# Kernel optimization log

Measured on AMD Instinct MI355X. Metric: run time of the kernel, lower is better.

## Reference

```python
import jax, jax.numpy as jnp
import numpy as np

B, N, C = 4, 2048, 64   # batch, tokens, num_feat
HS = 512                # hidden_size
H = HS // C             # 8 heads, head_dim = C = 64
EPS = 1e-6


def _ln(x, g, b):
    m = x.mean(-1, keepdims=True)
    v = ((x - m) ** 2).mean(-1, keepdims=True)
    return (x - m) / jnp.sqrt(v + EPS) * g + b


def setup_inputs() -> dict:
    key = jax.random.key(0)
    ks = jax.random.split(key, 8)
    s = 0.02
    return {
        "x": jax.random.normal(ks[0], (B, N, C), jnp.float32),
        "g1": jnp.ones((C,), jnp.float32),
        "be1": jnp.zeros((C,), jnp.float32),
        "Wqkv": jax.random.normal(ks[1], (C, 3 * HS), jnp.float32) * s,
        "bqkv": jnp.zeros((3 * HS,), jnp.float32),
        "Wout": jax.random.normal(ks[2], (HS, C), jnp.float32) * s,
        "bout": jnp.zeros((C,), jnp.float32),
        "g2": jnp.ones((C,), jnp.float32),
        "be2": jnp.zeros((C,), jnp.float32),
        "W1": jax.random.normal(ks[3], (C, HS // 8), jnp.float32) * s,
        "b1": jax.random.normal(ks[4], (HS // 8,), jnp.float32) * 1e-6,
        "W2": jax.random.normal(ks[5], (HS // 8, C), jnp.float32) * s,
        "b2": jax.random.normal(ks[6], (C,), jnp.float32) * 1e-6,
    }


def reference(x, g1, be1, Wqkv, bqkv, Wout, bout, g2, be2, W1, b1, W2, b2):
    b_, n_, c_ = x.shape
    hs = Wout.shape[0]
    h_ = hs // c_
    res = x
    y = _ln(x, g1, be1)
    # fused QKV: (B,N,3*HS) -> (3,B,H,N,D) with D = c_
    qkv = (y @ Wqkv + bqkv).reshape(b_, n_, 3, h_, c_).transpose(2, 0, 3, 1, 4)
    q, k, v = qkv[0], qkv[1], qkv[2]
    scores = jnp.einsum('bhqd,bhkd->bhqk', q, k) / jnp.sqrt(jnp.asarray(c_, x.dtype))
    probs = jax.nn.softmax(scores, axis=-1)
    ctx = jnp.einsum('bhqk,bhkd->bhqd', probs, v)
    ctx = ctx.transpose(0, 2, 1, 3).reshape(b_, n_, hs)
    attn = jax.nn.gelu(ctx @ Wout + bout, approximate=False)  # GELU after out proj per source
    x2 = attn + res
    y2 = _ln(x2, g2, be2)
    mlp = jax.nn.gelu(y2 @ W1 + b1, approximate=False) @ W2 + b2
    return mlp + x2
```

## Files before the change

kernel.cpp:

```cpp
#include <hip/hip_runtime.h>


#define NN 2048
#define CC 64
#define HH 8
#define HSZ 512
#define QKSCALE 0.42466092f

typedef __bf16 bf16x8 __attribute__((ext_vector_type(8)));
typedef float f32x4 __attribute__((ext_vector_type(4)));

__device__ __forceinline__ float b2f(unsigned short u) {
  union { unsigned int i; float f; } v; v.i = ((unsigned int)u) << 16; return v.f;
}
__device__ __forceinline__ unsigned short f2b(float f) {
  union { float f; unsigned int i; } v; v.f = f;
  unsigned int r = v.i + 0x7FFFu + ((v.i >> 16) & 1u);
  return (unsigned short)(r >> 16);
}
__device__ __forceinline__ unsigned int pk2(float a, float b) {
  return (unsigned int)f2b(a) | ((unsigned int)f2b(b) << 16);
}
__device__ __forceinline__ unsigned char f2fp8(float f) {
  int p = __builtin_amdgcn_cvt_pk_fp8_f32(f, f, 0, false);
  return (unsigned char)(p & 0xFF);
}
__device__ __forceinline__ float gelu_f(float x) {
  return 0.5f * x * (1.0f + erff(x * 0.7071067811865475f));
}

__global__ __launch_bounds__(256) void k_ln_qkv(
    const float* __restrict__ x,
    const float* __restrict__ g1,
    const float* __restrict__ be1,
    const float* __restrict__ W,
    const float* __restrict__ bqkv,
    unsigned char* __restrict__ Qb,
    unsigned char* __restrict__ Kb,
    unsigned char* __restrict__ VbT)
{
  __shared__ __align__(16) unsigned short As[64 * 72];
  __shared__ __align__(16) unsigned short Ws[128 * 72];
  const int tid = threadIdx.x, wv = tid >> 6, lane = tid & 63;
  const int col = lane & 15, quad = lane >> 4;
  const int bm = blockIdx.x & 127, bn = blockIdx.x >> 7;
  const int m0 = bm * 64, nw = bn * 128;

  const int c4 = tid & 15;
  float4 gv = *(const float4*)(g1 + c4 * 4);
  float4 bv = *(const float4*)(be1 + c4 * 4);
  #pragma unroll
  for (int s = 0; s < 4; ++s) {
    int idx = s * 256 + tid;
    int row = idx >> 4;
    float4 xv = *(const float4*)(x + (size_t)(m0 + row) * CC + c4 * 4);
    float ps = xv.x + xv.y + xv.z + xv.w;
    float ps2 = xv.x * xv.x + xv.y * xv.y + xv.z * xv.z + xv.w * xv.w;
    #pragma unroll
    for (int off = 8; off; off >>= 1) {
      ps += __shfl_xor(ps, off, 16);
      ps2 += __shfl_xor(ps2, off, 16);
    }
    float mean = ps * (1.0f / 64.0f);
    float var = ps2 * (1.0f / 64.0f) - mean * mean;
    float rs = rsqrtf(var + 1e-6f);
    uint2 packed;
    packed.x = pk2((xv.x - mean) * rs * gv.x + bv.x, (xv.y - mean) * rs * gv.y + bv.y);
    packed.y = pk2((xv.z - mean) * rs * gv.z + bv.z, (xv.w - mean) * rs * gv.w + bv.w);
    *(uint2*)&As[row * 72 + c4 * 4] = packed;
  }

  {
    const int c_loc = tid & 127;
    const int kg = tid >> 7;
    const int ng = nw + c_loc;
    #pragma unroll
    for (int g = 0; g < 4; ++g) {
      float wv8[8];
      #pragma unroll
      for (int j = 0; j < 8; ++j) wv8[j] = W[(size_t)(kg * 32 + g * 8 + j) * 1536 + ng];
      uint4 u;
      u.x = pk2(wv8[0], wv8[1]); u.y = pk2(wv8[2], wv8[3]);
      u.z = pk2(wv8[4], wv8[5]); u.w = pk2(wv8[6], wv8[7]);
      *(uint4*)&Ws[c_loc * 72 + kg * 32 + g * 8] = u;
    }
  }
  __syncthreads();

  bf16x8 af0 = *(const bf16x8*)&As[(wv * 16 + col) * 72 + quad * 8];
  bf16x8 af1 = *(const bf16x8*)&As[(wv * 16 + col) * 72 + 32 + quad * 8];

  f32x4 acc[8];
  #pragma unroll
  for (int nt = 0; nt < 8; ++nt) acc[nt] = (f32x4){0.f, 0.f, 0.f, 0.f};
  #pragma unroll
  for (int nt = 0; nt < 8; ++nt) {
    bf16x8 b0 = *(const bf16x8*)&Ws[(nt * 16 + col) * 72 + quad * 8];
    bf16x8 b1 = *(const bf16x8*)&Ws[(nt * 16 + col) * 72 + 32 + quad * 8];
    acc[nt] = __builtin_amdgcn_mfma_f32_16x16x32_bf16(af0, b0, acc[nt], 0, 0, 0);
    acc[nt] = __builtin_amdgcn_mfma_f32_16x16x32_bf16(af1, b1, acc[nt], 0, 0, 0);
  }

  const int tkb = m0 + wv * 16 + quad * 4;
  const int bb = tkb >> 11;
  const int nnb = tkb & 2047;
  #pragma unroll
  for (int nt = 0; nt < 8; ++nt) {
    const int n0 = nw + nt * 16;
    const int which = n0 >> 9;
    const int h = (n0 >> 6) & 7;
    const int d0 = n0 & 63;
    const float bias = bqkv[n0 + col];
    float vv[4];
    #pragma unroll
    for (int r = 0; r < 4; ++r) vv[r] = acc[nt][r] + bias;
    if (which == 2) {
      int lo = __builtin_amdgcn_cvt_pk_fp8_f32(vv[0], vv[1], 0, false);
      int full = __builtin_amdgcn_cvt_pk_fp8_f32(vv[2], vv[3], lo, true);
      *(unsigned int*)(VbT + ((size_t)(bb * HH + h) * CC + d0 + col) * NN + nnb) =
          (unsigned int)full;
    } else {
      unsigned char* dst = (which == 0) ? Qb : Kb;
      #pragma unroll
      for (int r = 0; r < 4; ++r)
        dst[((size_t)(bb * HH + h) * NN + nnb + r) * CC + d0 + col] =
            f2fp8(vv[r] * QKSCALE);
    }
  }
}

__global__ __launch_bounds__(256) void k_attn(
    const unsigned char* __restrict__ Q,
    const unsigned char* __restrict__ K,
    const unsigned char* __restrict__ VT,
    const float* __restrict__ Wout,
    unsigned short* __restrict__ part,
    float* __restrict__ lsums)
{
  __shared__ __align__(16) unsigned char smem[27648];
  unsigned char* Ks = smem;
  unsigned char* Vt = smem + 5120;
  unsigned short* Wb = (unsigned short*)smem;
  unsigned short* Ob = (unsigned short*)(smem + 9216);
  const int tid = threadIdx.x, wv = tid >> 6, lane = tid & 63;
  const int col = lane & 15, quad = lane >> 4;
  const int bid = blockIdx.x;
  const int tc = bid & 1, qc = (bid >> 1) & 15, bh = bid >> 5;
  const size_t base = (size_t)bh * NN * CC;
  const int q0 = qc * 128 + wv * 32;
  const int t0 = tc * 1024;

  long qf[2][2];
  #pragma unroll
  for (int mt = 0; mt < 2; ++mt)
    #pragma unroll
    for (int kh = 0; kh < 2; ++kh)
      qf[mt][kh] = *(const long*)(Q + base + (size_t)(q0 + mt * 16 + col) * CC + kh * 32 + quad * 8);

  f32x4 o[2][4];
  #pragma unroll
  for (int mt = 0; mt < 2; ++mt)
    #pragma unroll
    for (int dt = 0; dt < 4; ++dt) o[mt][dt] = (f32x4){0.f, 0.f, 0.f, 0.f};
  float ls[2] = {0.f, 0.f};
  const int sl0 = ((quad & 1) << 5) + col;
  const int sl1 = sl0 + 16;
  const bool hiq = (quad >= 2);

  for (int kt = 0; kt < 16; ++kt) {
    const int tb = t0 + kt * 64;
    {
      int row = tid >> 2, c16 = (tid & 3) << 4;
      *(uint4*)&Ks[row * 80 + c16] = *(const uint4*)(K + base + (size_t)(tb + row) * CC + c16);
      *(uint4*)&Vt[row * 80 + c16] = *(const uint4*)(VT + base + (size_t)row * NN + tb + c16);
    }
    __syncthreads();

    unsigned int Dw[2][4];
    #pragma unroll
    for (int ct = 0; ct < 4; ++ct) {
      long k0 = *(const long*)&Ks[(ct * 16 + col) * 80 + quad * 8];
      long k1 = *(const long*)&Ks[(ct * 16 + col) * 80 + 32 + quad * 8];
      #pragma unroll
      for (int mt = 0; mt < 2; ++mt) {
        f32x4 a = (f32x4){0.f, 0.f, 0.f, 0.f};
        a = __builtin_amdgcn_mfma_f32_16x16x32_fp8_fp8(k0, qf[mt][0], a, 0, 0, 0);
        a = __builtin_amdgcn_mfma_f32_16x16x32_fp8_fp8(k1, qf[mt][1], a, 0, 0, 0);
        float p0 = exp2f(a[0]), p1 = exp2f(a[1]);
        float p2 = exp2f(a[2]), p3 = exp2f(a[3]);
        ls[mt] += (p0 + p1) + (p2 + p3);
        int lo = __builtin_amdgcn_cvt_pk_fp8_f32(p0, p1, 0, false);
        Dw[mt][ct] = (unsigned int)__builtin_amdgcn_cvt_pk_fp8_f32(p2, p3, lo, true);
      }
    }

    #pragma unroll
    for (int kh = 0; kh < 2; ++kh) {
      long pb[2];
      #pragma unroll
      for (int mt = 0; mt < 2; ++mt) {
        unsigned int a0 = (unsigned int)__shfl((int)Dw[mt][2 * kh], sl0, 64);
        unsigned int b0 = (unsigned int)__shfl((int)Dw[mt][2 * kh + 1], sl0, 64);
        unsigned int a1 = (unsigned int)__shfl((int)Dw[mt][2 * kh], sl1, 64);
        unsigned int b1 = (unsigned int)__shfl((int)Dw[mt][2 * kh + 1], sl1, 64);
        unsigned long lo = hiq ? b0 : a0;
        unsigned long hi = hiq ? b1 : a1;
        pb[mt] = (long)(lo | (hi << 32));
      }
      #pragma unroll
      for (int dt = 0; dt < 4; ++dt) {
        long vf = *(const long*)&Vt[(dt * 16 + col) * 80 + kh * 32 + quad * 8];
        o[0][dt] = __builtin_amdgcn_mfma_f32_16x16x32_fp8_fp8(vf, pb[0], o[0][dt], 0, 0, 0);
        o[1][dt] = __builtin_amdgcn_mfma_f32_16x16x32_fp8_fp8(vf, pb[1], o[1][dt], 0, 0, 0);
      }
    }
    __syncthreads();
  }

  const int h = bh & 7, b = bh >> 3;
  #pragma unroll
  for (int mt = 0; mt < 2; ++mt) {
    float v = ls[mt];
    v += __shfl_xor(v, 16, 64);
    v += __shfl_xor(v, 32, 64);
    if (quad == 0)
      lsums[(size_t)(tc * 32 + bh) * NN + q0 + mt * 16 + col] = v;
  }

  {
    const int c = tid & 63, kg = tid >> 6;
    #pragma unroll
    for (int j = 0; j < 16; ++j)
      Wb[c * 72 + kg * 16 + j] = f2b(Wout[(size_t)(h * 64 + kg * 16 + j) * 64 + c]);
  }
  unsigned short* Obw = Ob + wv * (32 * 72);
  #pragma unroll
  for (int mt = 0; mt < 2; ++mt)
    #pragma unroll
    for (int dt = 0; dt < 4; ++dt) {
      uint2 u;
      u.x = pk2(o[mt][dt][0], o[mt][dt][1]);
      u.y = pk2(o[mt][dt][2], o[mt][dt][3]);
      *(uint2*)&Obw[(mt * 16 + col) * 72 + dt * 16 + quad * 4] = u;
    }
  __syncthreads();

  #pragma unroll
  for (int mt = 0; mt < 2; ++mt) {
    bf16x8 oa0 = *(const bf16x8*)&Obw[(mt * 16 + col) * 72 + quad * 8];
    bf16x8 oa1 = *(const bf16x8*)&Obw[(mt * 16 + col) * 72 + 32 + quad * 8];
    #pragma unroll
    for (int nt = 0; nt < 4; ++nt) {
      bf16x8 bw0 = *(const bf16x8*)&Wb[(nt * 16 + col) * 72 + quad * 8];
      bf16x8 bw1 = *(const bf16x8*)&Wb[(nt * 16 + col) * 72 + 32 + quad * 8];
      f32x4 ac = (f32x4){0.f, 0.f, 0.f, 0.f};
      ac = __builtin_amdgcn_mfma_f32_16x16x32_bf16(oa0, bw0, ac, 0, 0, 0);
      ac = __builtin_amdgcn_mfma_f32_16x16x32_bf16(oa1, bw1, ac, 0, 0, 0);
      #pragma unroll
      for (int r = 0; r < 4; ++r) {
        int n = q0 + mt * 16 + quad * 4 + r;
        part[((size_t)(tc * 32 + bh) * NN + n) * CC + nt * 16 + col] = f2b(ac[r]);
      }
    }
  }
}

__global__ __launch_bounds__(256) void k_post(
    const unsigned short* __restrict__ part,
    const float* __restrict__ lsums,
    const float* __restrict__ x,
    const float* __restrict__ bout,
    const float* __restrict__ g2,
    const float* __restrict__ be2,
    const float* __restrict__ W1,
    const float* __restrict__ b1,
    const float* __restrict__ W2,
    const float* __restrict__ b2v,
    float* __restrict__ out)
{
  __shared__ __align__(16) float Ws1[64 * 64];
  __shared__ __align__(16) float Ws2[64 * 64];
  __shared__ float ys[4][64], hs[4][64];
  const int tid = threadIdx.x, wid = tid >> 6, lane = tid & 63;
  const int tk = blockIdx.x * 4 + wid;
  const int b = tk >> 11, n = tk & 2047;

  #pragma unroll
  for (int p = 0; p < 4; ++p) {
    int idx = p * 256 + tid;
    *(float4*)&Ws1[idx * 4] = *(const float4*)(W1 + idx * 4);
    *(float4*)&Ws2[idx * 4] = *(const float4*)(W2 + idx * 4);
  }

  float proj = 0.f;
  #pragma unroll
  for (int h = 0; h < 8; ++h) {
    size_t i0 = (size_t)(b * HH + h) * NN + n;
    size_t i1 = i0 + (size_t)32 * NN;
    float p = b2f(part[i0 * CC + lane]) + b2f(part[i1 * CC + lane]);
    float l = lsums[i0] + lsums[i1];
    proj += p * __builtin_amdgcn_rcpf(l);
  }

  float a = gelu_f(proj + bout[lane]);
  float x2 = a + x[(size_t)tk * CC + lane];
  float s = x2;
  #pragma unroll
  for (int off = 32; off; off >>= 1) s += __shfl_xor(s, off, 64);
  float mean = s * (1.0f / 64.0f);
  float d = x2 - mean;
  float vs = d * d;
  #pragma unroll
  for (int off = 32; off; off >>= 1) vs += __shfl_xor(vs, off, 64);
  float var = vs * (1.0f / 64.0f);
  ys[wid][lane] = d * rsqrtf(var + 1e-6f) * g2[lane] + be2[lane];
  __syncthreads();

  float acc2 = 0.f;
  #pragma unroll 8
  for (int c = 0; c < 64; ++c) acc2 += ys[wid][c] * Ws1[c * 64 + lane];
  hs[wid][lane] = gelu_f(acc2 + b1[lane]);

  float acc3 = 0.f;
  #pragma unroll 8
  for (int c = 0; c < 64; ++c) acc3 += hs[wid][c] * Ws2[c * 64 + lane];
  out[(size_t)tk * CC + lane] = acc3 + b2v[lane] + x2;
}

extern "C" void kernel_launch(void* const* d_in, const int* in_sizes, int n_in,
                              void* d_out, int out_size, void* d_ws, size_t ws_size,
                              hipStream_t stream) {
  const float* x    = (const float*)d_in[0];
  const float* g1   = (const float*)d_in[1];
  const float* be1  = (const float*)d_in[2];
  const float* Wqkv = (const float*)d_in[3];
  const float* bqkv = (const float*)d_in[4];
  const float* Wout = (const float*)d_in[5];
  const float* bout = (const float*)d_in[6];
  const float* g2   = (const float*)d_in[7];
  const float* be2  = (const float*)d_in[8];
  const float* W1   = (const float*)d_in[9];
  const float* b1   = (const float*)d_in[10];
  const float* W2   = (const float*)d_in[11];
  const float* b2   = (const float*)d_in[12];
  float* out = (float*)d_out;

  unsigned char* wsb = (unsigned char*)d_ws;
  const size_t SZ = (size_t)4 * HH * NN * CC;
  unsigned char* Qb   = wsb;
  unsigned char* Kb   = wsb + SZ;
  unsigned char* VbT  = wsb + 2 * SZ;
  unsigned short* part = (unsigned short*)(wsb + 3 * SZ);
  float* lsums         = (float*)(wsb + 3 * SZ + 4 * SZ);

  k_ln_qkv<<<1536, 256, 0, stream>>>(x, g1, be1, Wqkv, bqkv, Qb, Kb, VbT);
  k_attn<<<1024, 256, 0, stream>>>(Qb, Kb, VbT, Wout, part, lsums);
  k_post<<<2048, 256, 0, stream>>>(part, lsums, x, bout, g2, be2, W1, b1, W2, b2, out);
}
```

Measured before the change: 163.9 us.

## Compute softmax row sums via extra MFMA with ones tile, batch two tokens per wave in post

Replaces the per-lane scalar accumulation of exp values (and its cross-lane shuffle reduction) with an extra fp8 MFMA against a ones row padded into the V tile in LDS, so the row sum falls out of the matrix unit. Swaps exp2f for the raw hardware exp2 builtin. In the post kernel each wave now processes two tokens, halving the grid and reusing each weight load from LDS for two accumulators. The row sum is now computed from fp8-quantized probabilities, which changes numerics slightly, and the LDS region past the V tile must fit in the shared buffer.

```diff
diff --git a/kernel.cpp b/kernel.cpp
--- a/kernel.cpp
+++ b/kernel.cpp
@@ -150,6 +150,12 @@
   const int q0 = qc * 128 + wv * 32;
   const int t0 = tc * 1024;
 
+  if (tid < 80) {
+    unsigned int fill = (tid < 5) ? 0x38383838u : 0u;
+    uint4 u; u.x = fill; u.y = fill; u.z = fill; u.w = fill;
+    *(uint4*)&Vt[64 * 80 + tid * 16] = u;
+  }
+
   long qf[2][2];
   #pragma unroll
   for (int mt = 0; mt < 2; ++mt)
@@ -158,11 +164,13 @@
       qf[mt][kh] = *(const long*)(Q + base + (size_t)(q0 + mt * 16 + col) * CC + kh * 32 + quad * 8);
 
   f32x4 o[2][4];
-  #pragma unroll
-  for (int mt = 0; mt < 2; ++mt)
+  f32x4 ol[2];
+  #pragma unroll
+  for (int mt = 0; mt < 2; ++mt) {
     #pragma unroll
     for (int dt = 0; dt < 4; ++dt) o[mt][dt] = (f32x4){0.f, 0.f, 0.f, 0.f};
-  float ls[2] = {0.f, 0.f};
+    ol[mt] = (f32x4){0.f, 0.f, 0.f, 0.f};
+  }
   const int sl0 = ((quad & 1) << 5) + col;
   const int sl1 = sl0 + 16;
   const bool hiq = (quad >= 2);
@@ -186,9 +194,10 @@
         f32x4 a = (f32x4){0.f, 0.f, 0.f, 0.f};
         a = __builtin_amdgcn_mfma_f32_16x16x32_fp8_fp8(k0, qf[mt][0], a, 0, 0, 0);
         a = __builtin_amdgcn_mfma_f32_16x16x32_fp8_fp8(k1, qf[mt][1], a, 0, 0, 0);
-        float p0 = exp2f(a[0]), p1 = exp2f(a[1]);
-        float p2 = exp2f(a[2]), p3 = exp2f(a[3]);
-        ls[mt] += (p0 + p1) + (p2 + p3);
+        float p0 = __builtin_amdgcn_exp2f(a[0]);
+        float p1 = __builtin_amdgcn_exp2f(a[1]);
+        float p2 = __builtin_amdgcn_exp2f(a[2]);
+        float p3 = __builtin_amdgcn_exp2f(a[3]);
         int lo = __builtin_amdgcn_cvt_pk_fp8_f32(p0, p1, 0, false);
         Dw[mt][ct] = (unsigned int)__builtin_amdgcn_cvt_pk_fp8_f32(p2, p3, lo, true);
       }
@@ -213,6 +222,9 @@
         o[0][dt] = __builtin_amdgcn_mfma_f32_16x16x32_fp8_fp8(vf, pb[0], o[0][dt], 0, 0, 0);
         o[1][dt] = __builtin_amdgcn_mfma_f32_16x16x32_fp8_fp8(vf, pb[1], o[1][dt], 0, 0, 0);
       }
+      long vl = *(const long*)&Vt[(64 + col) * 80 + kh * 32 + quad * 8];
+      ol[0] = __builtin_amdgcn_mfma_f32_16x16x32_fp8_fp8(vl, pb[0], ol[0], 0, 0, 0);
+      ol[1] = __builtin_amdgcn_mfma_f32_16x16x32_fp8_fp8(vl, pb[1], ol[1], 0, 0, 0);
     }
     __syncthreads();
   }
@@ -220,11 +232,8 @@
   const int h = bh & 7, b = bh >> 3;
   #pragma unroll
   for (int mt = 0; mt < 2; ++mt) {
-    float v = ls[mt];
-    v += __shfl_xor(v, 16, 64);
-    v += __shfl_xor(v, 32, 64);
     if (quad == 0)
-      lsums[(size_t)(tc * 32 + bh) * NN + q0 + mt * 16 + col] = v;
+      lsums[(size_t)(tc * 32 + bh) * NN + q0 + mt * 16 + col] = ol[mt][0];
   }
 
   {
@@ -280,10 +289,10 @@
 {
   __shared__ __align__(16) float Ws1[64 * 64];
   __shared__ __align__(16) float Ws2[64 * 64];
-  __shared__ float ys[4][64], hs[4][64];
+  __shared__ float ys[8][64], hs[8][64];
   const int tid = threadIdx.x, wid = tid >> 6, lane = tid & 63;
-  const int tk = blockIdx.x * 4 + wid;
-  const int b = tk >> 11, n = tk & 2047;
+  const int w2 = wid * 2;
+  const int tk0 = blockIdx.x * 8 + w2;
 
   #pragma unroll
   for (int p = 0; p < 4; ++p) {
@@ -292,39 +301,60 @@
     *(float4*)&Ws2[idx * 4] = *(const float4*)(W2 + idx * 4);
   }
 
-  float proj = 0.f;
-  #pragma unroll
-  for (int h = 0; h < 8; ++h) {
-    size_t i0 = (size_t)(b * HH + h) * NN + n;
-    size_t i1 = i0 + (size_t)32 * NN;
-    float p = b2f(part[i0 * CC + lane]) + b2f(part[i1 * CC + lane]);
-    float l = lsums[i0] + lsums[i1];
-    proj += p * __builtin_amdgcn_rcpf(l);
-  }
-
-  float a = gelu_f(proj + bout[lane]);
-  float x2 = a + x[(size_t)tk * CC + lane];
-  float s = x2;
-  #pragma unroll
-  for (int off = 32; off; off >>= 1) s += __shfl_xor(s, off, 64);
-  float mean = s * (1.0f / 64.0f);
-  float d = x2 - mean;
-  float vs = d * d;
-  #pragma unroll
-  for (int off = 32; off; off >>= 1) vs += __shfl_xor(vs, off, 64);
-  float var = vs * (1.0f / 64.0f);
-  ys[wid][lane] = d * rsqrtf(var + 1e-6f) * g2[lane] + be2[lane];
+  const float boutl = bout[lane];
+  const float g2l = g2[lane], be2l = be2[lane];
+  float x2v[2];
+  #pragma unroll
+  for (int t = 0; t < 2; ++t) {
+    const int tk = tk0 + t;
+    const int b = tk >> 11, n = tk & 2047;
+    float proj = 0.f;
+    #pragma unroll
+    for (int h = 0; h < 8; ++h) {
+      size_t i0 = (size_t)(b * HH + h) * NN + n;
+      size_t i1 = i0 + (size_t)32 * NN;
+      float p = b2f(part[i0 * CC + lane]) + b2f(part[i1 * CC + lane]);
+      float l = lsums[i0] + lsums[i1];
+      proj += p * __builtin_amdgcn_rcpf(l);
+    }
+    float a = gelu_f(proj + boutl);
+    float x2 = a + x[(size_t)tk * CC + lane];
+    x2v[t] = x2;
+    float s = x2;
+    #pragma unroll
+    for (int off = 32; off; off >>= 1) s += __shfl_xor(s, off, 64);
+    float mean = s * (1.0f / 64.0f);
+    float d = x2 - mean;
+    float vs = d * d;
+    #pragma unroll
+    for (int off = 32; off; off >>= 1) vs += __shfl_xor(vs, off, 64);
+    float var = vs * (1.0f / 64.0f);
+    ys[w2 + t][lane] = d * rsqrtf(var + 1e-6f) * g2l + be2l;
+  }
   __syncthreads();
 
-  float acc2 = 0.f;
+  float acc2[2] = {0.f, 0.f};
   #pragma unroll 8
-  for (int c = 0; c < 64; ++c) acc2 += ys[wid][c] * Ws1[c * 64 + lane];
-  hs[wid][lane] = gelu_f(acc2 + b1[lane]);
-
-  float acc3 = 0.f;
+  for (int c = 0; c < 64; ++c) {
+    float w = Ws1[c * 64 + lane];
+    acc2[0] += ys[w2][c] * w;
+    acc2[1] += ys[w2 + 1][c] * w;
+  }
+  const float b1l = b1[lane];
+  hs[w2][lane] = gelu_f(acc2[0] + b1l);
+  hs[w2 + 1][lane] = gelu_f(acc2[1] + b1l);
+
+  float acc3[2] = {0.f, 0.f};
   #pragma unroll 8
-  for (int c = 0; c < 64; ++c) acc3 += hs[wid][c] * Ws2[c * 64 + lane];
-  out[(size_t)tk * CC + lane] = acc3 + b2v[lane] + x2;
+  for (int c = 0; c < 64; ++c) {
+    float w = Ws2[c * 64 + lane];
+    acc3[0] += hs[w2][c] * w;
+    acc3[1] += hs[w2 + 1][c] * w;
+  }
+  const float b2l = b2v[lane];
+  #pragma unroll
+  for (int t = 0; t < 2; ++t)
+    out[(size_t)(tk0 + t) * CC + lane] = acc3[t] + b2l + x2v[t];
 }
 
 extern "C" void kernel_launch(void* const* d_in, const int* in_sizes, int n_in,
@@ -355,5 +385,5 @@
 
   k_ln_qkv<<<1536, 256, 0, stream>>>(x, g1, be1, Wqkv, bqkv, Qb, Kb, VbT);
   k_attn<<<1024, 256, 0, stream>>>(Qb, Kb, VbT, Wout, part, lsums);
-  k_post<<<2048, 256, 0, stream>>>(part, lsums, x, bout, g2, be2, W1, b1, W2, b2, out);
-}
+  k_post<<<1024, 256, 0, stream>>>(part, lsums, x, bout, g2, be2, W1, b1, W2, b2, out);
+}
```

After: 152.3 us. 7.1% less time.
